# Optimization experiments

Measured on AMD Instinct MI355X. Metric: run time of the kernel, lower is better.

Reference implementation:

```python
import jax, jax.numpy as jnp
import numpy as np


def _mingru_scan(xp, wz, bz, wh, bh):
    # minGRU step_parallel with h0 = 0 (torch parallel_scan drops b[:,0]):
    #   z = sigmoid(W_z x), h_tilde = W_h x, a = 1-z
    #   H_t = sum_{s<=t} (z_s * h_tilde_s) * prod_{r<s} a_r
    z = jax.nn.sigmoid(xp @ wz + bz)          # (B, L, H)
    h_tilde = xp @ wh + bh                    # (B, L, H)  (no tanh in step_parallel)
    a = 1.0 - z
    A = jnp.cumprod(a, axis=1)                # (B, L, H)
    A_shift = jnp.concatenate([jnp.ones_like(A[:, :1]), A[:, :-1]], axis=1)
    return jnp.cumsum(z * h_tilde * A_shift, axis=1)


def setup_inputs() -> dict:
    B, L, H, T = 8, 4096, 512, 8
    key = jax.random.key(0)
    ks = jax.random.split(key, 18)

    def w(k, shape, fan_in):
        lim = 1.0 / np.sqrt(fan_in)
        return jax.random.uniform(k, shape, jnp.float32, -lim, lim)

    inp = {
        "x": jax.random.normal(ks[0], (B, L, 2), dtype=jnp.float32),
        "t": jax.random.uniform(ks[1], (B, L), dtype=jnp.float32),
        # time_enc: Linear(1,8) -> ReLU -> Linear(8,8); stored as (in,out)
        "te_w1": w(ks[2], (1, T), 1), "te_b1": w(ks[3], (T,), 1),
        "te_w2": w(ks[4], (T, T), T), "te_b2": w(ks[5], (T,), T),
        # input projections: Linear(2+8, H)
        "fproj_w": w(ks[6], (2 + T, H), 2 + T), "fproj_b": w(ks[7], (H,), 2 + T),
        "bproj_w": w(ks[8], (2 + T, H), 2 + T), "bproj_b": w(ks[9], (H,), 2 + T),
        # minGRU cells: W_z, W_h Linear(H, H)
        "f_wz": w(ks[10], (H, H), H), "f_bz": w(ks[11], (H,), H),
        "f_wh": w(ks[12], (H, H), H), "f_bh": w(ks[13], (H,), H),
        "b_wz": w(ks[14], (H, H), H), "b_bz": w(ks[15], (H,), H),
        "b_wh": w(ks[16], (H, H), H), "b_bh": w(ks[17], (H,), H),
    }
    return inp


def reference(x, t, te_w1, te_b1, te_w2, te_b2,
              fproj_w, fproj_b, bproj_w, bproj_b,
              f_wz, f_bz, f_wh, f_bh,
              b_wz, b_bz, b_wh, b_bh):
    # time encoding on shifted times
    t_shifted = (t - t[:, :1])[..., None]                     # (B, L, 1)
    t_enc = jax.nn.relu(t_shifted @ te_w1 + te_b1) @ te_w2 + te_b2  # (B, L, 8)
    xc = jnp.concatenate([x, t_enc], axis=-1)                 # (B, L, 10)

    # forward direction: scan, then shift right by one (h_t holds state BEFORE step t)
    hf = _mingru_scan(xc @ fproj_w + fproj_b, f_wz, f_bz, f_wh, f_bh)
    zeros = jnp.zeros_like(hf[:, :1])
    h_fwd = jnp.concatenate([zeros, hf[:, :-1]], axis=1)

    # backward direction: flip, scan, flip back, shift left by one
    hb = _mingru_scan(jnp.flip(xc, axis=1) @ bproj_w + bproj_b, b_wz, b_bz, b_wh, b_bh)
    hb = jnp.flip(hb, axis=1)
    h_bwd = jnp.concatenate([hb[:, 1:], zeros], axis=1)

    return (t_enc, h_fwd, h_bwd)
```

## Files before the change

### kernel.cpp

```cpp
#include <hip/hip_runtime.h>
#include <hip/hip_bf16.h>
#include <stdint.h>

#define BB   8
#define LSEQ 4096
#define HH   512
#define KIN  10
#define NC   32
#define CHK  128
#define KT   16
#define KC   (HH/KT)
#define XPAD 12

#define OUT_TENC_N (BB*LSEQ*8)
#define HSIZE      ((size_t)BB*LSEQ*HH)

#define WOFF_WEFF 0
#define WOFF_BEFF 20480
#define WOFF_SG   22528
#define WOFF_SP   (WOFF_SG + 2*BB*NC*HH)
#define WOFF_XC   (WOFF_SP + 2*BB*NC*HH)
#define WS_FLOATS (WOFF_XC + BB*LSEQ*XPAD)
#define POFF_W    WOFF_SG
#define POFF_B    (WOFF_SG + 4*KT*KIN*HH)

__global__ __launch_bounds__(512)
void compose1(const float* __restrict__ fproj_w, const float* __restrict__ fproj_b,
              const float* __restrict__ bproj_w, const float* __restrict__ bproj_b,
              const float* __restrict__ f_wz, const float* __restrict__ f_wh,
              const float* __restrict__ b_wz, const float* __restrict__ b_wh,
              float* __restrict__ ws) {
    const int m  = blockIdx.x;
    const int kt = blockIdx.y;
    const int j  = threadIdx.x;
    const float* P  = (m < 2) ? fproj_w : bproj_w;
    const float* pb = (m < 2) ? fproj_b : bproj_b;
    const float* W  = (m == 0) ? f_wz : (m == 1) ? f_wh : (m == 2) ? b_wz : b_wh;

    float acc[KIN];
    #pragma unroll
    for (int i = 0; i < KIN; i++) acc[i] = 0.f;
    float accb = 0.f;
    #pragma unroll 4
    for (int kk = 0; kk < KC; kk++) {
        const int k = kt * KC + kk;
        float w = W[(size_t)k*HH + j];
        accb = fmaf(pb[k], w, accb);
        #pragma unroll
        for (int i = 0; i < KIN; i++) acc[i] = fmaf(P[(size_t)i*HH + k], w, acc[i]);
    }
    const int mt = m*KT + kt;
    #pragma unroll
    for (int i = 0; i < KIN; i++) ws[POFF_W + ((size_t)mt*KIN + i)*HH + j] = acc[i];
    ws[POFF_B + (size_t)mt*HH + j] = accb;
}

__global__ __launch_bounds__(512)
void compose2(const float* __restrict__ f_bz, const float* __restrict__ f_bh,
              const float* __restrict__ b_bz, const float* __restrict__ b_bh,
              float* __restrict__ ws) {
    const int m = blockIdx.x, j = threadIdx.x;
    const float* wb = (m == 0) ? f_bz : (m == 1) ? f_bh : (m == 2) ? b_bz : b_bh;
    #pragma unroll
    for (int i = 0; i < KIN; i++) {
        float s = 0.f;
        #pragma unroll
        for (int kt = 0; kt < KT; kt++)
            s += ws[POFF_W + ((size_t)(m*KT + kt)*KIN + i)*HH + j];
        ws[WOFF_WEFF + (m*KIN + i)*HH + j] = s;
    }
    float sb = wb[j];
    #pragma unroll
    for (int kt = 0; kt < KT; kt++) sb += ws[POFF_B + (size_t)(m*KT + kt)*HH + j];
    ws[WOFF_BEFF + m*HH + j] = sb;
}

__global__ __launch_bounds__(256)
void xc_kernel(const float* __restrict__ x, const float* __restrict__ t,
               const float* __restrict__ te_w1, const float* __restrict__ te_b1,
               const float* __restrict__ te_w2, const float* __restrict__ te_b2,
               float* __restrict__ ws, float* __restrict__ out) {
    const int idx = blockIdx.x * 256 + threadIdx.x;
    const int b = idx >> 12;
    float ts = t[idx] - t[(size_t)b << 12];

    float h1[8];
    #pragma unroll
    for (int j = 0; j < 8; j++) h1[j] = fmaxf(0.f, fmaf(ts, te_w1[j], te_b1[j]));

    float o[8];
    #pragma unroll
    for (int j = 0; j < 8; j++) {
        float v = te_b2[j];
        #pragma unroll
        for (int k = 0; k < 8; k++) v = fmaf(h1[k], te_w2[k*8 + j], v);
        o[j] = v;
    }
    float4* ob = reinterpret_cast<float4*>(&out[(size_t)idx * 8]);
    ob[0] = make_float4(o[0], o[1], o[2], o[3]);
    ob[1] = make_float4(o[4], o[5], o[6], o[7]);
    float2 xv = reinterpret_cast<const float2*>(x)[idx];
    float4* xb = reinterpret_cast<float4*>(&ws[WOFF_XC + (size_t)idx * XPAD]);
    xb[0] = make_float4(xv.x, xv.y, o[0], o[1]);
    xb[1] = make_float4(o[2], o[3], o[4], o[5]);
    xb[2] = make_float4(o[6], o[7], 0.f, 0.f);
}

template<int EMIT>
__global__ __launch_bounds__(512)
void scan2(const float* __restrict__ weff, const float* __restrict__ beff,
           const float* __restrict__ xc,
           float* __restrict__ sg, float* __restrict__ sp,
           float* __restrict__ out) {
    const int c = blockIdx.x;
    const int b = blockIdx.y;
    const int d = blockIdx.z;
    const int h = threadIdx.x;

    float wz[KIN], wh[KIN];
    #pragma unroll
    for (int i = 0; i < KIN; i++) {
        wz[i] = weff[((2*d    )*KIN + i)*HH + h];
        wh[i] = weff[((2*d + 1)*KIN + i)*HH + h];
    }
    float bz = beff[(2*d    )*HH + h];
    float bh = beff[(2*d + 1)*HH + h];

    const int t0 = (d == 0) ? c * CHK : LSEQ - (c + 1) * CHK;
    const float* __restrict__ xr = xc + ((size_t)b * LSEQ + t0) * XPAD;

    float Hacc = 0.f, Pr = 1.f;
    if (EMIT) {
        const float* g = sg + (size_t)((d*BB + b)*NC)*HH + h;
        const float* p = sp + (size_t)((d*BB + b)*NC)*HH + h;
        for (int cc = 0; cc < c; cc++) {
            Hacc = fmaf(Pr, g[(size_t)cc*HH], Hacc);
            Pr  *= p[(size_t)cc*HH];
        }
    }

    float* ob = out + OUT_TENC_N + (size_t)d * HSIZE + (size_t)b * LSEQ * HH + h;
    for (int tt = 0; tt < CHK; tt++) {
        const int row = (d == 0) ? tt : (CHK - 1 - tt);
        const float* q = xr + row * XPAD;
        float zp = bz, hp = bh;
        #pragma unroll
        for (int i = 0; i < KIN; i++) {
            float v = q[i];
            zp = fmaf(v, wz[i], zp);
            hp = fmaf(v, wh[i], hp);
        }
        float z = __builtin_amdgcn_rcpf(1.f + __expf(-zp));
        if (EMIT)
            ob[(size_t)(t0 + row) * HH] = Hacc;
        Hacc = fmaf(Pr, z * hp, Hacc);
        Pr *= (1.f - z);
    }

    if (!EMIT) {
        sg[(size_t)((d*BB + b)*NC + c)*HH + h] = Hacc;
        sp[(size_t)((d*BB + b)*NC + c)*HH + h] = Pr;
    }
}

__global__ __launch_bounds__(256)
void scan_serial(const float* __restrict__ x, const float* __restrict__ t,
                 const float* __restrict__ te_w1, const float* __restrict__ te_b1,
                 const float* __restrict__ te_w2, const float* __restrict__ te_b2,
                 const float* __restrict__ PWf, const float* __restrict__ PBf,
                 const float* __restrict__ PWb, const float* __restrict__ PBb,
                 const float* __restrict__ f_wz, const float* __restrict__ f_bz,
                 const float* __restrict__ f_wh, const float* __restrict__ f_bh,
                 const float* __restrict__ b_wz, const float* __restrict__ b_bz,
                 const float* __restrict__ b_wh, const float* __restrict__ b_bh,
                 float* __restrict__ out) {
    const int hg = blockIdx.x, b = blockIdx.y, d = blockIdx.z;
    const int h = hg * 256 + threadIdx.x;
    const float* PW = d ? PWb : PWf;   const float* PB = d ? PBb : PBf;
    const float* WZ = d ? b_wz : f_wz; const float* BZ = d ? b_bz : f_bz;
    const float* WH = d ? b_wh : f_wh; const float* BH = d ? b_bh : f_bh;

    float wz[KIN], wh[KIN];
    #pragma unroll
    for (int i = 0; i < KIN; i++) { wz[i] = 0.f; wh[i] = 0.f; }
    float bz = BZ[h], bh = BH[h];
    for (int k = 0; k < HH; k++) {
        float vz = WZ[k*HH + h], vh = WH[k*HH + h], pbk = PB[k];
        bz = fmaf(pbk, vz, bz);  bh = fmaf(pbk, vh, bh);
        #pragma unroll
        for (int i = 0; i < KIN; i++) {
            wz[i] = fmaf(PW[i*HH + k], vz, wz[i]);
            wh[i] = fmaf(PW[i*HH + k], vh, wh[i]);
        }
    }
    __shared__ float w2s[64], w1s[8], b1s[8], b2s[8], xcs[256*KIN];
    if (threadIdx.x < 64) w2s[threadIdx.x] = te_w2[threadIdx.x];
    if (threadIdx.x < 8) {
        w1s[threadIdx.x] = te_w1[threadIdx.x];
        b1s[threadIdx.x] = te_b1[threadIdx.x];
        b2s[threadIdx.x] = te_b2[threadIdx.x];
    }
    const float t_b0 = t[(size_t)b * LSEQ];
    float Hacc = 0.f, Pr = 1.f;
    float* ob = out + OUT_TENC_N + (size_t)d*HSIZE + (size_t)b*LSEQ*HH + h;
    for (int cc = 0; cc < LSEQ/256; cc++) {
        const int t0 = (d == 0) ? cc*256 : LSEQ - (cc+1)*256;
        __syncthreads();
        {
            const size_t gi = (size_t)b*LSEQ + t0 + threadIdx.x;
            float ts = t[gi] - t_b0;
            float h1[8];
            #pragma unroll
            for (int j = 0; j < 8; j++) h1[j] = fmaxf(0.f, fmaf(ts, w1s[j], b1s[j]));
            float* xr = &xcs[threadIdx.x * KIN];
            float2 xv = reinterpret_cast<const float2*>(x)[gi];
            xr[0] = xv.x; xr[1] = xv.y;
            #pragma unroll
            for (int j = 0; j < 8; j++) {
                float v = b2s[j];
                #pragma unroll
                for (int k = 0; k < 8; k++) v = fmaf(h1[k], w2s[k*8+j], v);
                xr[2+j] = v;
            }
        }
        __syncthreads();
        for (int tt = 0; tt < 256; tt++) {
            const int row = (d == 0) ? tt : (255 - tt);
            const float* xr = &xcs[row * KIN];
            float zp = bz, hp = bh;
            #pragma unroll
            for (int i = 0; i < KIN; i++) { zp = fmaf(xr[i], wz[i], zp); hp = fmaf(xr[i], wh[i], hp); }
            float z = __builtin_amdgcn_rcpf(1.f + __expf(-zp));
            ob[(size_t)(t0 + row) * HH] = Hacc;
            Hacc = fmaf(Pr, z * hp, Hacc);
            Pr *= (1.f - z);
        }
    }
}

__global__ __launch_bounds__(256)
void tenc_fb(const float* __restrict__ t,
             const float* __restrict__ te_w1, const float* __restrict__ te_b1,
             const float* __restrict__ te_w2, const float* __restrict__ te_b2,
             float* __restrict__ out) {
    int idx = blockIdx.x * 256 + threadIdx.x;
    int b = idx >> 12;
    float ts = t[idx] - t[(size_t)b << 12];
    float h1[8];
    #pragma unroll
    for (int j = 0; j < 8; j++) h1[j] = fmaxf(0.f, fmaf(ts, te_w1[j], te_b1[j]));
    float o[8];
    #pragma unroll
    for (int j = 0; j < 8; j++) {
        float v = te_b2[j];
        #pragma unroll
        for (int k = 0; k < 8; k++) v = fmaf(h1[k], te_w2[k*8 + j], v);
        o[j] = v;
    }
    float4* ob = reinterpret_cast<float4*>(&out[(size_t)idx * 8]);
    ob[0] = make_float4(o[0], o[1], o[2], o[3]);
    ob[1] = make_float4(o[4], o[5], o[6], o[7]);
}

extern "C" void kernel_launch(void* const* d_in, const int* in_sizes, int n_in,
                              void* d_out, int out_size, void* d_ws, size_t ws_size,
                              hipStream_t stream) {
    const float* x       = (const float*)d_in[0];
    const float* t       = (const float*)d_in[1];
    const float* te_w1   = (const float*)d_in[2];
    const float* te_b1   = (const float*)d_in[3];
    const float* te_w2   = (const float*)d_in[4];
    const float* te_b2   = (const float*)d_in[5];
    const float* fproj_w = (const float*)d_in[6];
    const float* fproj_b = (const float*)d_in[7];
    const float* bproj_w = (const float*)d_in[8];
    const float* bproj_b = (const float*)d_in[9];
    const float* f_wz    = (const float*)d_in[10];
    const float* f_bz    = (const float*)d_in[11];
    const float* f_wh    = (const float*)d_in[12];
    const float* f_bh    = (const float*)d_in[13];
    const float* b_wz    = (const float*)d_in[14];
    const float* b_bz    = (const float*)d_in[15];
    const float* b_wh    = (const float*)d_in[16];
    const float* b_bh    = (const float*)d_in[17];
    float* out           = (float*)d_out;
    float* ws            = (float*)d_ws;

    if (ws_size >= (size_t)WS_FLOATS * sizeof(float)) {
        xc_kernel<<<(BB*LSEQ)/256, 256, 0, stream>>>(x, t, te_w1, te_b1, te_w2, te_b2, ws, out);
        dim3 gc(4, KT);
        compose1<<<gc, 512, 0, stream>>>(fproj_w, fproj_b, bproj_w, bproj_b,
                                         f_wz, f_wh, b_wz, b_wh, ws);
        compose2<<<4, 512, 0, stream>>>(f_bz, f_bh, b_bz, b_bh, ws);

        dim3 g(NC, BB, 2);
        scan2<0><<<g, 512, 0, stream>>>(ws + WOFF_WEFF, ws + WOFF_BEFF, ws + WOFF_XC,
                                        ws + WOFF_SG, ws + WOFF_SP, out);
        scan2<1><<<g, 512, 0, stream>>>(ws + WOFF_WEFF, ws + WOFF_BEFF, ws + WOFF_XC,
                                        ws + WOFF_SG, ws + WOFF_SP, out);
    } else {
        tenc_fb<<<(BB*LSEQ)/256, 256, 0, stream>>>(t, te_w1, te_b1, te_w2, te_b2, out);
        dim3 g(2, BB, 2);
        scan_serial<<<g, 256, 0, stream>>>(x, t, te_w1, te_b1, te_w2, te_b2,
                                           fproj_w, fproj_b, bproj_w, bproj_b,
                                           f_wz, f_bz, f_wh, f_bh,
                                           b_wz, b_bz, b_wh, b_bh, out);
    }
}
```

Before: 261.9 us.

## Double chunk count and unroll scan by four with vectorized input loads

Halves the chunk length and doubles the number of chunks, so the chunked scan launches twice as many blocks and has a shorter serial loop per thread. The inner time loop is unrolled by four, loading four padded input rows with float4 reads and computing the gate values before the dependent accumulation chain. This aims to raise occupancy and instruction-level parallelism. In exchange, the EMIT pass must serially combine up to twice as many chunk prefixes, and the q[48] array adds register pressure.

New measurement: 282.0 us. 1.08x slower.

```diff
diff --git a/kernel.cpp b/kernel.cpp
--- a/kernel.cpp
+++ b/kernel.cpp
@@ -6,8 +6,8 @@
 #define LSEQ 4096
 #define HH   512
 #define KIN  10
-#define NC   32
-#define CHK  128
+#define NC   64
+#define CHK  64
 #define KT   16
 #define KC   (HH/KT)
 #define XPAD 12
@@ -123,11 +123,11 @@
         wz[i] = weff[((2*d    )*KIN + i)*HH + h];
         wh[i] = weff[((2*d + 1)*KIN + i)*HH + h];
     }
-    float bz = beff[(2*d    )*HH + h];
-    float bh = beff[(2*d + 1)*HH + h];
+    const float bz = beff[(2*d    )*HH + h];
+    const float bh = beff[(2*d + 1)*HH + h];
 
     const int t0 = (d == 0) ? c * CHK : LSEQ - (c + 1) * CHK;
-    const float* __restrict__ xr = xc + ((size_t)b * LSEQ + t0) * XPAD;
+    const float* __restrict__ xrc = xc + ((size_t)b * LSEQ + t0) * XPAD;
 
     float Hacc = 0.f, Pr = 1.f;
     if (EMIT) {
@@ -140,21 +140,39 @@
     }
 
     float* ob = out + OUT_TENC_N + (size_t)d * HSIZE + (size_t)b * LSEQ * HH + h;
-    for (int tt = 0; tt < CHK; tt++) {
-        const int row = (d == 0) ? tt : (CHK - 1 - tt);
-        const float* q = xr + row * XPAD;
-        float zp = bz, hp = bh;
-        #pragma unroll
-        for (int i = 0; i < KIN; i++) {
-            float v = q[i];
-            zp = fmaf(v, wz[i], zp);
-            hp = fmaf(v, wh[i], hp);
-        }
-        float z = __builtin_amdgcn_rcpf(1.f + __expf(-zp));
-        if (EMIT)
-            ob[(size_t)(t0 + row) * HH] = Hacc;
-        Hacc = fmaf(Pr, z * hp, Hacc);
-        Pr *= (1.f - z);
+
+    for (int s4 = 0; s4 < CHK; s4 += 4) {
+        const int mbase = (d == 0) ? s4 : (CHK - 4 - s4);
+        const float* qb = xrc + (size_t)mbase * XPAD;
+        float q[48];
+        #pragma unroll
+        for (int i = 0; i < 12; i++)
+            reinterpret_cast<float4*>(q)[i] = reinterpret_cast<const float4*>(qb)[i];
+
+        float g4[4], a4[4];
+        #pragma unroll
+        for (int u = 0; u < 4; u++) {
+            const int mi = (d == 0) ? u : (3 - u);
+            const float* r = q + mi * 12;
+            float zp = bz, hp = bh;
+            #pragma unroll
+            for (int i = 0; i < KIN; i++) {
+                zp = fmaf(r[i], wz[i], zp);
+                hp = fmaf(r[i], wh[i], hp);
+            }
+            float z = __builtin_amdgcn_rcpf(1.f + __expf(-zp));
+            g4[u] = z * hp;
+            a4[u] = 1.f - z;
+        }
+        #pragma unroll
+        for (int u = 0; u < 4; u++) {
+            if (EMIT) {
+                const int trow = (d == 0) ? (s4 + u) : (CHK - 1 - s4 - u);
+                ob[(size_t)(t0 + trow) * HH] = Hacc;
+            }
+            Hacc = fmaf(Pr, g4[u], Hacc);
+            Pr *= a4[u];
+        }
     }
 
     if (!EMIT) {
```
